# Optimization experiments

Hardware: AMD Instinct MI355X
Metric: run time of the kernel (lower is better)

Reference implementation:

```python
import jax, jax.numpy as jnp
import numpy as np
from jax import lax

B_SZ, D_SPEC, P, NC, MLP_D = 4096, 30, 9, 64, 64
L = P * P + 1  # 82 tokens (81 spiral + cls)


def _spiral_idx(patch=P):
    # Replicates Scan.forward's hardcoded assignments_map: center pixel, then
    # concentric rings (top row, right col, bottom row, left col), each of length 2r.
    cen = patch // 2
    rows, cols = [cen], [cen]
    for r in range(1, cen + 1):
        rows += [cen - r] * (2 * r); cols += list(range(cen - r + 1, cen + r + 1))
        rows += list(range(cen - r + 1, cen + r + 1)); cols += [cen + r] * (2 * r)
        rows += [cen + r] * (2 * r); cols += list(range(cen - r, cen + r))
        rows += list(range(cen - r, cen + r)); cols += [cen - r] * (2 * r)
    return np.asarray(rows), np.asarray(cols)

_ROWS, _COLS = _spiral_idx()


def _ln(x, g, b, eps=1e-5):
    m = x.mean(-1, keepdims=True)
    v = ((x - m) ** 2).mean(-1, keepdims=True)
    return (x - m) * lax.rsqrt(v + eps) * g + b


def _bn(x, g, b, m, v, nspatial, eps=1e-5):
    sh = (1, -1) + (1,) * nspatial
    return (x - m.reshape(sh)) * lax.rsqrt(v.reshape(sh) + eps) * g.reshape(sh) + b.reshape(sh)


def setup_inputs():
    key = jax.random.key(0)
    ks = iter(jax.random.split(key, 40))
    def rn(shape, s=0.1):
        return s * jax.random.normal(next(ks), shape, jnp.float32)
    return {
        "input_data": jax.random.normal(next(ks), (B_SZ, 1, D_SPEC, P, P), jnp.float32),
        "w3": rn((8, 1, 3, 3, 3)), "b3": rn((8,)),
        "g3": 1.0 + rn((8,)), "be3": rn((8,)), "m3": jnp.zeros((8,)), "v3": jnp.ones((8,)),
        "w2c": rn((NC, 8 * D_SPEC, 3, 3)), "b2c": rn((NC,)),
        "g2": 1.0 + rn((NC,)), "be2": rn((NC,)), "m2": jnp.zeros((NC,)), "v2": jnp.ones((NC,)),
        "pos_emb": rn((1, L, NC)), "cls_tok": rn((1, 1, NC)),
        "ln1_g": jnp.ones((NC,)), "ln1_b": jnp.zeros((NC,)),
        "Wb": rn((NC, NC)), "bb": rn((NC,)),
        "Wc": rn((NC, NC)), "bc": rn((NC,)),
        "Wd": rn((NC, NC)), "bd": rn((NC,)),
        "delta_p": rn((1, L, NC)), "A_p": rn((L, NC)),
        "Wst": rn((NC, NC)), "bst": rn((NC,)), "bias_st": rn((1, 1, NC)),
        "ln2_g": jnp.ones((NC,)), "ln2_b": jnp.zeros((NC,)),
        "Wm1": rn((NC, MLP_D)), "bm1": rn((MLP_D,)),
        "Wm2": rn((MLP_D, NC)), "bm2": rn((NC,)),
    }


def _forward(input_data, w3, b3, g3, be3, m3, v3, w2c, b2c, g2, be2, m2, v2,
             pos_emb, cls_tok, ln1_g, ln1_b, Wb, bb, Wc, bc, Wd, bd,
             delta_p, A_p, Wst, bst, bias_st, ln2_g, ln2_b, Wm1, bm1, Wm2, bm2):
    b = input_data.shape[0]
    # conv3d (SAME, k=3) + BN(eval) + ReLU
    h = lax.conv_general_dilated(input_data, w3, (1, 1, 1), [(1, 1)] * 3,
                                 dimension_numbers=("NCDHW", "OIDHW", "NCDHW"))
    h = jax.nn.relu(_bn(h + b3[None, :, None, None, None], g3, be3, m3, v3, 3))
    h = h.reshape(b, 8 * D_SPEC, P, P)  # 'b c h w y -> b (c h) w y'
    # conv2d (SAME, k=3) + BN(eval) + ReLU
    h = lax.conv_general_dilated(h, w2c, (1, 1), [(1, 1)] * 2,
                                 dimension_numbers=("NCHW", "OIHW", "NCHW"))
    h = jax.nn.relu(_bn(h + b2c[None, :, None, None], g2, be2, m2, v2, 2))
    # spiral scan gather: [B,C,H,W] -> [B,81,C]
    seq = jnp.transpose(h, (0, 2, 3, 1))[:, _ROWS, _COLS, :]
    tok = jnp.concatenate([jnp.broadcast_to(cls_tok, (b, 1, NC)), seq], axis=1) + pos_emb
    # (emb dropout = identity in eval)
    # --- Residual(LayerNormalize(S6_noC)) ---
    xn = _ln(tok, ln1_g, ln1_b)
    z = jax.nn.sigmoid(xn)
    B0 = xn @ Wb + bb
    C_ = xn @ Wc + bc
    sq = jnp.mean(xn, axis=1, keepdims=True)              # SToken squeeze [B,1,D]
    sq = jax.nn.sigmoid(jax.nn.relu(sq @ Wst + bst))
    T_ = (sq + bias_st) * xn                              # [B,L,D]
    delta = jax.nn.sigmoid(xn @ Wd + bd + delta_p)
    A_ = delta * A_p[None]                                # [B,L,D]
    Bx = delta * B0 * xn                                  # B_ * x fused
    def step(s, inp):
        a, bx, c, t = inp
        s = a * s + bx
        return s, c * s + t
    ins = (jnp.moveaxis(A_, 1, 0), jnp.moveaxis(Bx, 1, 0),
           jnp.moveaxis(C_, 1, 0), jnp.moveaxis(T_, 1, 0))  # [L,B,D]
    _, out = lax.scan(step, jnp.zeros((b, NC), xn.dtype), ins)
    tok = tok + jnp.moveaxis(out, 0, 1) * z               # residual
    # AdaptiveAvgPool1d(1) over seq + squeeze -> [B, D]
    pooled = tok.mean(axis=1)
    # --- Residual(LayerNormalize(MLP_Block)) (dropout = identity) ---
    yn = _ln(pooled, ln2_g, ln2_b)
    mlp = jax.nn.gelu(yn @ Wm1 + bm1, approximate=False) @ Wm2 + bm2
    return pooled + mlp


def reference(input_data, w3, b3, g3, be3, m3, v3, w2c, b2c, g2, be2, m2, v2,
              pos_emb, cls_tok, ln1_g, ln1_b, Wb, bb, Wc, bc, Wd, bd,
              delta_p, A_p, Wst, bst, bias_st, ln2_g, ln2_b, Wm1, bm1, Wm2, bm2):
    return _forward(input_data, w3, b3, g3, be3, m3, v3, w2c, b2c, g2, be2, m2, v2,
                    pos_emb, cls_tok, ln1_g, ln1_b, Wb, bb, Wc, bc, Wd, bd,
                    delta_p, A_p, Wst, bst, bias_st, ln2_g, ln2_b, Wm1, bm1, Wm2, bm2)
```

## Files before the change

kernel.cpp:

```cpp
#include <hip/hip_runtime.h>

typedef unsigned short u16;
typedef __attribute__((ext_vector_type(8))) short bf16x8;
typedef __attribute__((ext_vector_type(4))) float f32x4;
typedef __attribute__((ext_vector_type(4))) int i32x4;

#define DEV __device__ __forceinline__

DEV u16 f2bf(float f){
  unsigned u = __float_as_uint(f);
  u += 0x7fffu + ((u >> 16) & 1u);
  return (u16)(u >> 16);
}
DEV float bf2f(u16 h){ return __uint_as_float(((unsigned)h) << 16); }

DEV int spiral_t(int pix){
  int px = pix / 9, py = pix % 9;
  int dr = px - 4, dc = py - 4;
  int ar = dr < 0 ? -dr : dr, ac = dc < 0 ? -dc : dc;
  int r = ar > ac ? ar : ac;
  if (r == 0) return 0;
  int start = 1 + 4*r*(r-1);
  if (dr == -r && dc >= -r+1) return start + dc + r - 1;
  if (dc == r)  return start + 2*r + dr + r - 1;
  if (dr == r)  return start + 4*r + dc + r;
  return start + 6*r + dr + r;
}

__global__ __launch_bounds__(256) void k_wt(const float* __restrict__ w2c,
                                            const float* __restrict__ g2,
                                            const float* __restrict__ v2,
                                            u16* __restrict__ Wt2){
  int idx = blockIdx.x*256 + threadIdx.x;
  if (idx >= 72*64*32) return;
  int kk = idx & 31;
  int o  = (idx >> 5) & 63;
  int tile = idx >> 11;
  int dxy = tile >> 3;
  int chunk = tile & 7;
  int ch = chunk*32 + kk;
  float v = 0.f;
  if (ch < 240){
    float s2 = g2[o] * rsqrtf(v2[o] + 1e-5f);
    v = w2c[(o*240 + ch)*9 + dxy] * s2;
  }
  Wt2[idx] = f2bf(v);
}

__global__ __launch_bounds__(256) void k_conv3d(const float* __restrict__ x,
    const float* __restrict__ w3, const float* __restrict__ b3,
    const float* __restrict__ g3, const float* __restrict__ be3,
    const float* __restrict__ m3, const float* __restrict__ v3,
    u16* __restrict__ h1){
  __shared__ float tile[3872];
  __shared__ float wle[216];
  __shared__ float sc[8], sh[8];
  int b = blockIdx.x, tid = threadIdx.x;
  for (int i = tid; i < 3872; i += 256) tile[i] = 0.f;
  if (tid < 216) wle[tid] = w3[tid];
  if (tid < 8){
    float s = g3[tid]*rsqrtf(v3[tid]+1e-5f);
    sc[tid] = s;
    sh[tid] = (b3[tid]-m3[tid])*s + be3[tid];
  }
  __syncthreads();
  const float* xin = x + b*2430;
  for (int i = tid; i < 2430; i += 256){
    int dd = i / 81, rem = i % 81;
    int px = rem / 9, py = rem % 9;
    tile[(dd+1)*121 + (px+1)*11 + (py+1)] = xin[i];
  }
  __syncthreads();
  u16* hb = h1 + (size_t)b*19440;
  for (int p = tid; p < 2430; p += 256){
    int pix = p / 30, dd = p % 30;
    int px = pix / 9, py = pix % 9;
    const float* tp = tile + dd*121 + px*11 + py;
    float v[27];
    #pragma unroll
    for (int kd=0;kd<3;kd++)
      #pragma unroll
      for (int kx=0;kx<3;kx++)
        #pragma unroll
        for (int ky=0;ky<3;ky++)
          v[(kd*3+kx)*3+ky] = tp[kd*121 + kx*11 + ky];
    u16* hp = hb + pix*240 + dd;
    #pragma unroll
    for (int co=0;co<8;co++){
      float acc = 0.f;
      const float* wp = wle + co*27;
      #pragma unroll
      for (int q=0;q<27;q++) acc = fmaf(v[q], wp[q], acc);
      hp[co*30] = f2bf(fmaxf(acc*sc[co] + sh[co], 0.f));
    }
  }
}

__global__ __launch_bounds__(256, 2) void k_conv2d(const u16* __restrict__ h1,
    const u16* __restrict__ Wt2,
    const float* __restrict__ b2c, const float* __restrict__ g2,
    const float* __restrict__ be2, const float* __restrict__ m2,
    const float* __restrict__ v2,
    const float* __restrict__ pos_emb, const float* __restrict__ cls_tok,
    const float* __restrict__ ln1_g, const float* __restrict__ ln1_b,
    const float* __restrict__ Wst, const float* __restrict__ bst,
    const float* __restrict__ bias_st,
    u16* __restrict__ xn, float* __restrict__ tsum, float* __restrict__ sqs){
  __shared__ __align__(16) char smem[80848];
  const int ZROW = 80352;
  int tid = threadIdx.x;
  int wv = tid >> 6, ln = tid & 63;
  int lq = ln >> 4, lr = ln & 15;
  int img0 = blockIdx.x*2;
  size_t grow0 = (size_t)img0*81;

  for (int r = tid; r < 162; r += 256)
    *(i32x4*)(smem + r*496 + 480) = (i32x4){0,0,0,0};
  if (tid < 31) *(i32x4*)(smem + ZROW + tid*16) = (i32x4){0,0,0,0};
  {
    const u16* src = h1 + grow0*240;
    for (int idx = tid; idx < 162*30; idx += 256){
      int r = idx / 30, c = idx % 30;
      *(i32x4*)(smem + r*496 + c*16) = *(const i32x4*)(src + idx*8);
    }
  }
  __syncthreads();

  f32x4 acc[3][4];
  #pragma unroll
  for (int i=0;i<3;i++)
    #pragma unroll
    for (int j=0;j<4;j++) acc[i][j] = (f32x4){0.f,0.f,0.f,0.f};

  int bln = lr*32 + lq*8;

#define CALCADDR(TAP, A0, A1, A13)                                              \
  { int dx = (TAP)/3 - 1, dy = (TAP)%3 - 1;                                     \
    _Pragma("unroll")                                                           \
    for (int rt=0;rt<3;rt++){                                                   \
      int row = (wv*3+rt)*16 + lr;                                              \
      int pix = row % 81;                                                       \
      int px = pix/9, py = pix%9;                                               \
      int px2 = px + dx, py2 = py + dy;                                         \
      bool valid = (row < 162) && ((unsigned)px2 < 9u) && ((unsigned)py2 < 9u); \
      int nrow = (row - pix) + px2*9 + py2;                                     \
      int base = valid ? nrow*496 : ZROW;                                       \
      A0[rt]  = base + lq*16;                                                   \
      A1[rt]  = base + 64 + lq*16;                                              \
      A13[rt] = (lq == 3) ? ZROW : (A1[rt] + 384);                              \
    } }

#define LOADB(TAP, C, B)                                                        \
    { const u16* Bt_ = Wt2 + (TAP)*16384 + bln;                                 \
      _Pragma("unroll")                                                         \
      for (int kk=0;kk<2;kk++)                                                  \
        _Pragma("unroll")                                                       \
        for (int j=0;j<4;j++)                                                   \
          B[kk][j] = *(const bf16x8*)(Bt_ + ((C)*2+kk)*2048 + j*512); }

#define LOADA(C, SA0, SA1, SA13, A0, A1)                                        \
    { _Pragma("unroll")                                                         \
      for (int rt=0;rt<3;rt++){                                                 \
        A0[rt] = *(const bf16x8*)(smem + SA0[rt] + (C)*128);                    \
        A1[rt] = *(const bf16x8*)(smem + ((C)==3 ? SA13[rt]                     \
                                                 : SA1[rt] + (C)*128)); } }

#define DOMFMA(B, A0, A1)                                                       \
    { _Pragma("unroll")                                                         \
      for (int rt=0;rt<3;rt++)                                                  \
        _Pragma("unroll")                                                       \
        for (int j=0;j<4;j++)                                                   \
          acc[rt][j] = __builtin_amdgcn_mfma_f32_16x16x32_bf16(A0[rt], B[0][j], acc[rt][j], 0, 0, 0); \
      _Pragma("unroll")                                                         \
      for (int rt=0;rt<3;rt++)                                                  \
        _Pragma("unroll")                                                       \
        for (int j=0;j<4;j++)                                                   \
          acc[rt][j] = __builtin_amdgcn_mfma_f32_16x16x32_bf16(A1[rt], B[1][j], acc[rt][j], 0, 0, 0); }

  int aC0[3], aC1[3], aC13[3];
  int aN0[3], aN1[3], aN13[3];
  bf16x8 bX[2][4], bY[2][4], aX0[3], aX1[3], aY0[3], aY1[3];

  CALCADDR(0, aC0, aC1, aC13);
  LOADB(0, 0, bX); LOADA(0, aC0, aC1, aC13, aX0, aX1);
  LOADB(0, 1, bY); LOADA(1, aC0, aC1, aC13, aY0, aY1);

  for (int tap = 0; tap < 9; tap++){
    int ntap = (tap < 8) ? tap + 1 : 8;
    DOMFMA(bX, aX0, aX1);
    LOADB(tap, 2, bX); LOADA(2, aC0, aC1, aC13, aX0, aX1);
    DOMFMA(bY, aY0, aY1);
    LOADB(tap, 3, bY); LOADA(3, aC0, aC1, aC13, aY0, aY1);
    CALCADDR(ntap, aN0, aN1, aN13);
    DOMFMA(bX, aX0, aX1);
    LOADB(ntap, 0, bX); LOADA(0, aN0, aN1, aN13, aX0, aX1);
    DOMFMA(bY, aY0, aY1);
    LOADB(ntap, 1, bY); LOADA(1, aN0, aN1, aN13, aY0, aY1);
    #pragma unroll
    for (int rt=0;rt<3;rt++){ aC0[rt]=aN0[rt]; aC1[rt]=aN1[rt]; aC13[rt]=aN13[rt]; }
  }
#undef CALCADDR
#undef LOADB
#undef LOADA
#undef DOMFMA

  __syncthreads();

  float t2c[4], lg[4], lb[4];
  #pragma unroll
  for (int j=0;j<4;j++){
    int col = j*16 + lr;
    float s2 = g2[col]*rsqrtf(v2[col]+1e-5f);
    t2c[j] = (b2c[col]-m2[col])*s2 + be2[col];
    lg[j] = ln1_g[col]; lb[j] = ln1_b[col];
  }

  float st0[4]={0,0,0,0}, st1[4]={0,0,0,0};
  float sx0[4]={0,0,0,0}, sx1[4]={0,0,0,0};

  #pragma unroll
  for (int rt=0;rt<3;rt++){
    #pragma unroll
    for (int e=0;e<4;e++){
      int row = (wv*3+rt)*16 + lq*4 + e;
      if (row < 162){
        int im = (row >= 81);
        int pix = row - im*81;
        int tsp = spiral_t(pix);
        const float* pe = pos_emb + (1+tsp)*64;
        float y[4], m1 = 0.f, m2v = 0.f;
        #pragma unroll
        for (int j=0;j<4;j++){
          y[j] = fmaxf(acc[rt][j][e] + t2c[j], 0.f) + pe[j*16+lr];
          m1 += y[j]; m2v = fmaf(y[j], y[j], m2v);
        }
        #pragma unroll
        for (int off=1; off<16; off<<=1){
          m1  += __shfl_xor(m1,  off, 64);
          m2v += __shfl_xor(m2v, off, 64);
        }
        float mean = m1*(1.f/64.f);
        float var  = m2v*(1.f/64.f) - mean*mean;
        float rs = rsqrtf(var + 1e-5f);
        u16* dst = xn + ((size_t)(img0+im)*82 + 1 + tsp)*64;
        #pragma unroll
        for (int j=0;j<4;j++){
          float xnv = (y[j]-mean)*rs*lg[j] + lb[j];
          dst[j*16+lr] = f2bf(xnv);
          if (im == 0){ st0[j] += y[j]; sx0[j] += xnv; }
          else        { st1[j] += y[j]; sx1[j] += xnv; }
        }
      }
    }
  }

  #pragma unroll
  for (int j=0;j<4;j++){
    st0[j] += __shfl_xor(st0[j],16,64); st0[j] += __shfl_xor(st0[j],32,64);
    st1[j] += __shfl_xor(st1[j],16,64); st1[j] += __shfl_xor(st1[j],32,64);
    sx0[j] += __shfl_xor(sx0[j],16,64); sx0[j] += __shfl_xor(sx0[j],32,64);
    sx1[j] += __shfl_xor(sx1[j],16,64); sx1[j] += __shfl_xor(sx1[j],32,64);
  }
  float* partT = (float*)smem;
  float* partX = (float*)(smem + 2048);
  float* xsumL = (float*)(smem + 4096);
  if (lq == 0){
    #pragma unroll
    for (int j=0;j<4;j++){
      partT[wv*128 +       j*16+lr] = st0[j];
      partT[wv*128 + 64  + j*16+lr] = st1[j];
      partX[wv*128 +       j*16+lr] = sx0[j];
      partX[wv*128 + 64  + j*16+lr] = sx1[j];
    }
  }
  __syncthreads();
  if (tid < 128){
    int im = tid >> 6, d = tid & 63;
    float tt = partT[im*64+d] + partT[128+im*64+d] + partT[256+im*64+d] + partT[384+im*64+d];
    float xx = partX[im*64+d] + partX[128+im*64+d] + partX[256+im*64+d] + partX[384+im*64+d];
    float clsv = cls_tok[d] + pos_emb[d];
    float c1 = clsv, c2 = clsv*clsv;
    #pragma unroll
    for (int off=1; off<64; off<<=1){ c1 += __shfl_xor(c1, off, 64); c2 += __shfl_xor(c2, off, 64); }
    float cm = c1*(1.f/64.f), cv = c2*(1.f/64.f) - cm*cm;
    float cxn = (clsv - cm)*rsqrtf(cv + 1e-5f)*ln1_g[d] + ln1_b[d];
    xn[((size_t)(img0+im)*82)*64 + d] = f2bf(cxn);
    tsum[(size_t)(img0+im)*64 + d] = tt + clsv;
    xsumL[im*64 + d] = (xx + cxn) * (1.f/82.f);
  }
  __syncthreads();
  if (tid < 128){
    int im = tid >> 6, d = tid & 63;
    float a = bst[d];
    for (int k=0;k<64;k++) a = fmaf(xsumL[im*64+k], Wst[k*64+d], a);
    a = fmaxf(a, 0.f);
    a = 1.f/(1.f + __expf(-a));
    sqs[(size_t)(img0+im)*64 + d] = a + bias_st[d];
  }
}

__global__ __launch_bounds__(256, 1) void k_bcd(const u16* __restrict__ xn,
    const float* __restrict__ Wb, const float* __restrict__ Wc, const float* __restrict__ Wd,
    const float* __restrict__ bbv, const float* __restrict__ bcv,
    const float* __restrict__ bdv,
    const float* __restrict__ delta_p, const float* __restrict__ A_p,
    u16* __restrict__ Ax, u16* __restrict__ Bxx, u16* __restrict__ Cx){
  __shared__ char At[16384];
  int tid = threadIdx.x;
  int wv = tid >> 6, ln = tid & 63;
  int lq = ln >> 4, lr = ln & 15;
  size_t r0 = (size_t)blockIdx.x * 128;

  {
    int row = tid >> 1, hh = tid & 1;
    const char* src = (const char*)xn + (r0 + row)*128 + hh*64;
    #pragma unroll
    for (int c=0;c<4;c++){
      i32x4 v = *(const i32x4*)(src + c*16);
      *(i32x4*)(At + row*128 + ((hh*64 + c*16) ^ ((row&7)<<4))) = v;
    }
  }

  bf16x8 bfr[2][12];
  #pragma unroll
  for (int kk=0;kk<2;kk++)
    #pragma unroll
    for (int j=0;j<12;j++){
      int c = j*16 + lr;
      const float* W = (c < 64) ? Wb : ((c < 128) ? Wc : Wd);
      int cc = c & 63;
      int k0 = kk*32 + lq*8;
      bf16x8 f;
      #pragma unroll
      for (int e=0;e<8;e++) f[e] = (short)f2bf(W[(k0+e)*64 + cc]);
      bfr[kk][j] = f;
    }
  __syncthreads();

  f32x4 acc[2][12];
  #pragma unroll
  for (int i=0;i<2;i++)
    #pragma unroll
    for (int j=0;j<12;j++) acc[i][j] = (f32x4){0.f,0.f,0.f,0.f};

  #pragma unroll
  for (int kk=0;kk<2;kk++){
    bf16x8 afr[2];
    #pragma unroll
    for (int i=0;i<2;i++){
      int row = wv*32 + i*16 + lr;
      afr[i] = *(const bf16x8*)(At + row*128 + ((kk*64 + lq*16) ^ ((row&7)<<4)));
    }
    #pragma unroll
    for (int i=0;i<2;i++)
      #pragma unroll
      for (int j=0;j<12;j++)
        acc[i][j] = __builtin_amdgcn_mfma_f32_16x16x32_bf16(afr[i], bfr[kk][j], acc[i][j], 0, 0, 0);
  }

  #pragma unroll
  for (int i=0;i<2;i++){
    #pragma unroll
    for (int e=0;e<4;e++){
      int row = wv*32 + i*16 + lq*4 + e;
      unsigned rr = (unsigned)(r0 + row);
      unsigned t = rr % 82u;
      #pragma unroll
      for (int j=0;j<4;j++){
        int d = j*16 + lr;
        float B0 = acc[i][j][e]   + bbv[d];
        float Cv = acc[i][j+4][e] + bcv[d];
        float Dr = acc[i][j+8][e] + bdv[d] + delta_p[t*64+d];
        float D  = 1.f/(1.f + __expf(-Dr));
        int byte = j*32 + lr*2;
        float xv = bf2f(*(const u16*)(At + row*128 + (byte ^ ((row&7)<<4))));
        size_t o = (size_t)rr*64 + d;
        Ax[o]  = f2bf(D * A_p[t*64+d]);
        Bxx[o] = f2bf(D * B0 * xv);
        Cx[o]  = f2bf(Cv);
      }
    }
  }
}

__global__ __launch_bounds__(256) void k_scan(const u16* __restrict__ xn,
    const u16* __restrict__ Ax, const u16* __restrict__ Bxx, const u16* __restrict__ Cx,
    const float* __restrict__ tsum, const float* __restrict__ sqs,
    const float* __restrict__ ln2_g, const float* __restrict__ ln2_b,
    const float* __restrict__ Wm1, const float* __restrict__ bm1,
    const float* __restrict__ Wm2, const float* __restrict__ bm2,
    float* __restrict__ out){
  int tid = threadIdx.x, wv = tid >> 6, d = tid & 63;
  int b = blockIdx.x*4 + wv;
  float sq = sqs[b*64 + d];
  float s = 0.f, racc = 0.f;
  size_t base = (size_t)b*82*64 + d;
  #pragma unroll 2
  for (int t = 0; t < 82; t++){
    float a  = bf2f(Ax[base]);
    float bx = bf2f(Bxx[base]);
    float c  = bf2f(Cx[base]);
    float xv = bf2f(xn[base]);
    s = fmaf(a, s, bx);
    float o = fmaf(c, s, sq*xv);
    float z = 1.f/(1.f + __expf(-xv));
    racc = fmaf(o, z, racc);
    base += 64;
  }
  float pooled = (tsum[b*64 + d] + racc) * (1.f/82.f);
  float s1 = pooled, s2v = pooled*pooled;
  #pragma unroll
  for (int off=32; off>0; off>>=1){ s1 += __shfl_xor(s1, off, 64); s2v += __shfl_xor(s2v, off, 64); }
  float mean = s1*(1.f/64.f), var = s2v*(1.f/64.f) - mean*mean;
  float yn = (pooled - mean)*rsqrtf(var + 1e-5f)*ln2_g[d] + ln2_b[d];
  float a1 = bm1[d];
  for (int k=0;k<64;k++) a1 = fmaf(__shfl(yn, k, 64), Wm1[k*64+d], a1);
  float hg = 0.5f*a1*(1.f + erff(a1*0.70710678118654752f));
  float a2 = bm2[d];
  for (int k=0;k<64;k++) a2 = fmaf(__shfl(hg, k, 64), Wm2[k*64+d], a2);
  out[b*64 + d] = pooled + a2;
}

extern "C" void kernel_launch(void* const* d_in, const int* in_sizes, int n_in,
                              void* d_out, int out_size, void* d_ws, size_t ws_size,
                              hipStream_t stream){
  const float* x       = (const float*)d_in[0];
  const float* w3      = (const float*)d_in[1];
  const float* b3      = (const float*)d_in[2];
  const float* g3      = (const float*)d_in[3];
  const float* be3     = (const float*)d_in[4];
  const float* m3      = (const float*)d_in[5];
  const float* v3      = (const float*)d_in[6];
  const float* w2c     = (const float*)d_in[7];
  const float* b2c     = (const float*)d_in[8];
  const float* g2      = (const float*)d_in[9];
  const float* be2     = (const float*)d_in[10];
  const float* m2      = (const float*)d_in[11];
  const float* v2      = (const float*)d_in[12];
  const float* pos_emb = (const float*)d_in[13];
  const float* cls_tok = (const float*)d_in[14];
  const float* ln1_g   = (const float*)d_in[15];
  const float* ln1_b   = (const float*)d_in[16];
  const float* Wb      = (const float*)d_in[17];
  const float* bbv     = (const float*)d_in[18];
  const float* Wc      = (const float*)d_in[19];
  const float* bc      = (const float*)d_in[20];
  const float* Wd      = (const float*)d_in[21];
  const float* bd      = (const float*)d_in[22];
  const float* delta_p = (const float*)d_in[23];
  const float* A_p     = (const float*)d_in[24];
  const float* Wst     = (const float*)d_in[25];
  const float* bst     = (const float*)d_in[26];
  const float* bias_st = (const float*)d_in[27];
  const float* ln2_g   = (const float*)d_in[28];
  const float* ln2_b   = (const float*)d_in[29];
  const float* Wm1     = (const float*)d_in[30];
  const float* bm1     = (const float*)d_in[31];
  const float* Wm2     = (const float*)d_in[32];
  const float* bm2     = (const float*)d_in[33];

  char* ws = (char*)d_ws;
  u16*   h1   = (u16*)ws;
  u16*   Wt2  = (u16*)(ws + 159252480);
  u16*   xnb  = (u16*)(ws + 159571968);
  float* tsum = (float*)(ws + 202563584);
  float* sqs  = (float*)(ws + 203612160);
  u16*   Ax   = (u16*)ws;
  u16*   Cx   = (u16*)(ws + 42991616);
  u16*   Bxx  = (u16*)(ws + 85983232);

  k_wt    <<<576,  256, 0, stream>>>(w2c, g2, v2, Wt2);
  k_conv3d<<<4096, 256, 0, stream>>>(x, w3, b3, g3, be3, m3, v3, h1);
  k_conv2d<<<2048, 256, 0, stream>>>(h1, Wt2, b2c, g2, be2, m2, v2,
                                     pos_emb, cls_tok, ln1_g, ln1_b,
                                     Wst, bst, bias_st, xnb, tsum, sqs);
  k_bcd   <<<2624, 256, 0, stream>>>(xnb, Wb, Wc, Wd, bbv, bc, bd, delta_p, A_p,
                                     Ax, Bxx, Cx);
  k_scan  <<<1024, 256, 0, stream>>>(xnb, Ax, Bxx, Cx, tsum, sqs,
                                     ln2_g, ln2_b, Wm1, bm1, Wm2, bm2, (float*)d_out);
}
```

Baseline: 412.4 us.

## Triple-buffer conv weight fragments, prioritize MFMA waves, split squeeze matvec

The implicit-GEMM conv2d main loop now rotates three B-fragment register buffers instead of two, so global weight loads for later K-chunks are issued earlier and have more MFMA work to hide behind. The loop is unrolled over groups of three taps, and the first weight loads are issued before the shared-memory fill. MFMA blocks are wrapped in s_setprio to favour waves doing matrix work. The squeeze matvec now uses all 256 threads, with each thread summing half of the k range and a shuffle combining the halves. The extra buffer raises VGPR pressure, which could hurt the 2-waves-per-SIMD occupancy target.

```diff
diff --git a/kernel.cpp b/kernel.cpp
--- a/kernel.cpp
+++ b/kernel.cpp
@@ -114,6 +114,21 @@
   int img0 = blockIdx.x*2;
   size_t grow0 = (size_t)img0*81;
 
+  int bln = lr*32 + lq*8;
+
+#define LOADB(TAP, C, B)                                                        \
+    { const u16* Bt_ = Wt2 + (TAP)*16384 + bln;                                 \
+      _Pragma("unroll")                                                         \
+      for (int kk=0;kk<2;kk++)                                                  \
+        _Pragma("unroll")                                                       \
+        for (int j=0;j<4;j++)                                                   \
+          B[kk][j] = *(const bf16x8*)(Bt_ + ((C)*2+kk)*2048 + j*512); }
+
+  bf16x8 bB0[2][4], bB1[2][4], bB2[2][4];
+  LOADB(0, 0, bB0);
+  LOADB(0, 1, bB1);
+  LOADB(0, 2, bB2);
+
   for (int r = tid; r < 162; r += 256)
     *(i32x4*)(smem + r*496 + 480) = (i32x4){0,0,0,0};
   if (tid < 31) *(i32x4*)(smem + ZROW + tid*16) = (i32x4){0,0,0,0};
@@ -131,8 +146,6 @@
   for (int i=0;i<3;i++)
     #pragma unroll
     for (int j=0;j<4;j++) acc[i][j] = (f32x4){0.f,0.f,0.f,0.f};
-
-  int bln = lr*32 + lq*8;
 
 #define CALCADDR(TAP, A0, A1, A13)                                              \
   { int dx = (TAP)/3 - 1, dy = (TAP)%3 - 1;                                     \
@@ -150,14 +163,6 @@
       A13[rt] = (lq == 3) ? ZROW : (A1[rt] + 384);                              \
     } }
 
-#define LOADB(TAP, C, B)                                                        \
-    { const u16* Bt_ = Wt2 + (TAP)*16384 + bln;                                 \
-      _Pragma("unroll")                                                         \
-      for (int kk=0;kk<2;kk++)                                                  \
-        _Pragma("unroll")                                                       \
-        for (int j=0;j<4;j++)                                                   \
-          B[kk][j] = *(const bf16x8*)(Bt_ + ((C)*2+kk)*2048 + j*512); }
-
 #define LOADA(C, SA0, SA1, SA13, A0, A1)                                        \
     { _Pragma("unroll")                                                         \
       for (int rt=0;rt<3;rt++){                                                 \
@@ -166,7 +171,8 @@
                                                  : SA1[rt] + (C)*128)); } }
 
 #define DOMFMA(B, A0, A1)                                                       \
-    { _Pragma("unroll")                                                         \
+    { __builtin_amdgcn_s_setprio(1);                                            \
+      _Pragma("unroll")                                                         \
       for (int rt=0;rt<3;rt++)                                                  \
         _Pragma("unroll")                                                       \
         for (int j=0;j<4;j++)                                                   \
@@ -175,34 +181,41 @@
       for (int rt=0;rt<3;rt++)                                                  \
         _Pragma("unroll")                                                       \
         for (int j=0;j<4;j++)                                                   \
-          acc[rt][j] = __builtin_amdgcn_mfma_f32_16x16x32_bf16(A1[rt], B[1][j], acc[rt][j], 0, 0, 0); }
+          acc[rt][j] = __builtin_amdgcn_mfma_f32_16x16x32_bf16(A1[rt], B[1][j], acc[rt][j], 0, 0, 0); \
+      __builtin_amdgcn_s_setprio(0); }
+
+#define TAPBODY(TAPV, BA, BB, BC)                                               \
+  { int ntap_ = (TAPV) < 8 ? (TAPV)+1 : 8;                                      \
+    DOMFMA(BA, aAX0, aAX1);                                                     \
+    LOADB((TAPV), 3, BA); LOADA(2, aC0, aC1, aC13, aAX0, aAX1);                 \
+    DOMFMA(BB, aAY0, aAY1);                                                     \
+    LOADB(ntap_, 0, BB); CALCADDR(ntap_, aN0, aN1, aN13);                       \
+    LOADA(3, aC0, aC1, aC13, aAY0, aAY1);                                       \
+    DOMFMA(BC, aAX0, aAX1);                                                     \
+    LOADB(ntap_, 1, BC); LOADA(0, aN0, aN1, aN13, aAX0, aAX1);                  \
+    DOMFMA(BA, aAY0, aAY1);                                                     \
+    LOADB(ntap_, 2, BA); LOADA(1, aN0, aN1, aN13, aAY0, aAY1);                  \
+    _Pragma("unroll")                                                           \
+    for (int rt=0;rt<3;rt++){ aC0[rt]=aN0[rt]; aC1[rt]=aN1[rt]; aC13[rt]=aN13[rt]; } }
 
   int aC0[3], aC1[3], aC13[3];
   int aN0[3], aN1[3], aN13[3];
-  bf16x8 bX[2][4], bY[2][4], aX0[3], aX1[3], aY0[3], aY1[3];
+  bf16x8 aAX0[3], aAX1[3], aAY0[3], aAY1[3];
 
   CALCADDR(0, aC0, aC1, aC13);
-  LOADB(0, 0, bX); LOADA(0, aC0, aC1, aC13, aX0, aX1);
-  LOADB(0, 1, bY); LOADA(1, aC0, aC1, aC13, aY0, aY1);
-
-  for (int tap = 0; tap < 9; tap++){
-    int ntap = (tap < 8) ? tap + 1 : 8;
-    DOMFMA(bX, aX0, aX1);
-    LOADB(tap, 2, bX); LOADA(2, aC0, aC1, aC13, aX0, aX1);
-    DOMFMA(bY, aY0, aY1);
-    LOADB(tap, 3, bY); LOADA(3, aC0, aC1, aC13, aY0, aY1);
-    CALCADDR(ntap, aN0, aN1, aN13);
-    DOMFMA(bX, aX0, aX1);
-    LOADB(ntap, 0, bX); LOADA(0, aN0, aN1, aN13, aX0, aX1);
-    DOMFMA(bY, aY0, aY1);
-    LOADB(ntap, 1, bY); LOADA(1, aN0, aN1, aN13, aY0, aY1);
-    #pragma unroll
-    for (int rt=0;rt<3;rt++){ aC0[rt]=aN0[rt]; aC1[rt]=aN1[rt]; aC13[rt]=aN13[rt]; }
+  LOADA(0, aC0, aC1, aC13, aAX0, aAX1);
+  LOADA(1, aC0, aC1, aC13, aAY0, aAY1);
+
+  for (int t3 = 0; t3 < 9; t3 += 3){
+    TAPBODY(t3+0, bB0, bB1, bB2);
+    TAPBODY(t3+1, bB1, bB2, bB0);
+    TAPBODY(t3+2, bB2, bB0, bB1);
   }
 #undef CALCADDR
 #undef LOADB
 #undef LOADA
 #undef DOMFMA
+#undef TAPBODY
 
   __syncthreads();
 
@@ -289,13 +302,20 @@
     xsumL[im*64 + d] = (xx + cxn) * (1.f/82.f);
   }
   __syncthreads();
-  if (tid < 128){
-    int im = tid >> 6, d = tid & 63;
-    float a = bst[d];
-    for (int k=0;k<64;k++) a = fmaf(xsumL[im*64+k], Wst[k*64+d], a);
-    a = fmaxf(a, 0.f);
-    a = 1.f/(1.f + __expf(-a));
-    sqs[(size_t)(img0+im)*64 + d] = a + bias_st[d];
+  {
+    int im = tid >> 7, d2 = tid & 127;
+    int d = d2 >> 1, half = d2 & 1;
+    float a = 0.f;
+    int k0 = half*32;
+    #pragma unroll
+    for (int k=0;k<32;k++) a = fmaf(xsumL[im*64 + k0+k], Wst[(k0+k)*64+d], a);
+    a += __shfl_xor(a, 1, 64);
+    if (half == 0){
+      a += bst[d];
+      a = fmaxf(a, 0.f);
+      a = 1.f/(1.f + __expf(-a));
+      sqs[(size_t)(img0+im)*64 + d] = a + bias_st[d];
+    }
   }
 }
 
```

After: 407.0 us. Within noise of the previous version (-1.3%).

## Split conv2d K across wave pairs with LDS reduction and setprio MFMA groups

Applied to the files above, without the earlier changes.

Restructures the conv2d MFMA loop so each pair of waves covers 96 rows (6 row tiles) and splits the 4 K-chunks of each tap between the two waves. Each wave then loads only half the weight fragments per tap, and the partial accumulators are reduced through shared memory before the epilogue. The loop interleaves per-tile LDS loads with MFMA groups and raises wave priority around the MFMAs. The final Wst matvec now uses all 256 threads, each summing half of K and combining with a shuffle. In exchange the kernel carries twice as many accumulator registers and an extra LDS exchange with barriers, which may hurt occupancy at 2 blocks per CU.

```diff
diff --git a/kernel.cpp b/kernel.cpp
--- a/kernel.cpp
+++ b/kernel.cpp
@@ -111,8 +111,24 @@
   int tid = threadIdx.x;
   int wv = tid >> 6, ln = tid & 63;
   int lq = ln >> 4, lr = ln & 15;
+  int p = wv >> 1, q = wv & 1;
   int img0 = blockIdx.x*2;
   size_t grow0 = (size_t)img0*81;
+
+  int bln = lr*32 + lq*8;
+  int c0 = q*2, c1 = q*2 + 1;
+
+#define LOADB(TAP, C, B)                                                        \
+    { const u16* Bt_ = Wt2 + (TAP)*16384 + bln;                                 \
+      _Pragma("unroll")                                                         \
+      for (int kk=0;kk<2;kk++)                                                  \
+        _Pragma("unroll")                                                       \
+        for (int j=0;j<4;j++)                                                   \
+          B[kk][j] = *(const bf16x8*)(Bt_ + ((C)*2+kk)*2048 + j*512); }
+
+  bf16x8 bA[2][4], bB[2][4];
+  LOADB(0, c0, bA);
+  LOADB(0, c1, bB);
 
   for (int r = tid; r < 162; r += 256)
     *(i32x4*)(smem + r*496 + 480) = (i32x4){0,0,0,0};
@@ -126,84 +142,90 @@
   }
   __syncthreads();
 
-  f32x4 acc[3][4];
-  #pragma unroll
-  for (int i=0;i<3;i++)
+  f32x4 acc[6][4];
+  #pragma unroll
+  for (int i=0;i<6;i++)
     #pragma unroll
     for (int j=0;j<4;j++) acc[i][j] = (f32x4){0.f,0.f,0.f,0.f};
 
-  int bln = lr*32 + lq*8;
-
-#define CALCADDR(TAP, A0, A1, A13)                                              \
+  int aC0[6], aC1[6];
+  bf16x8 afr[6][2];
+
+#define CALCADDR(TAP)                                                           \
   { int dx = (TAP)/3 - 1, dy = (TAP)%3 - 1;                                     \
     _Pragma("unroll")                                                           \
-    for (int rt=0;rt<3;rt++){                                                   \
-      int row = (wv*3+rt)*16 + lr;                                              \
+    for (int rt=0;rt<6;rt++){                                                   \
+      int row = p*96 + rt*16 + lr;                                              \
       int pix = row % 81;                                                       \
       int px = pix/9, py = pix%9;                                               \
       int px2 = px + dx, py2 = py + dy;                                         \
       bool valid = (row < 162) && ((unsigned)px2 < 9u) && ((unsigned)py2 < 9u); \
       int nrow = (row - pix) + px2*9 + py2;                                     \
       int base = valid ? nrow*496 : ZROW;                                       \
-      A0[rt]  = base + lq*16;                                                   \
-      A1[rt]  = base + 64 + lq*16;                                              \
-      A13[rt] = (lq == 3) ? ZROW : (A1[rt] + 384);                              \
+      aC0[rt] = base + lq*16;                                                   \
+      aC1[rt] = base + 64 + lq*16;                                              \
     } }
 
-#define LOADB(TAP, C, B)                                                        \
-    { const u16* Bt_ = Wt2 + (TAP)*16384 + bln;                                 \
-      _Pragma("unroll")                                                         \
-      for (int kk=0;kk<2;kk++)                                                  \
+#define LOADA1(RT, C)                                                           \
+    { afr[RT][0] = *(const bf16x8*)(smem + aC0[RT] + (C)*128);                  \
+      int a1a_ = ((C)==3) ? ((lq==3) ? ZROW : aC1[RT] + 384)                    \
+                          : (aC1[RT] + (C)*128);                                \
+      afr[RT][1] = *(const bf16x8*)(smem + a1a_); }
+
+#define GROUP(B, NC)                                                            \
+    { _Pragma("unroll")                                                         \
+      for (int rt=0;rt<6;rt++){                                                 \
+        __builtin_amdgcn_s_setprio(1);                                          \
         _Pragma("unroll")                                                       \
         for (int j=0;j<4;j++)                                                   \
-          B[kk][j] = *(const bf16x8*)(Bt_ + ((C)*2+kk)*2048 + j*512); }
-
-#define LOADA(C, SA0, SA1, SA13, A0, A1)                                        \
-    { _Pragma("unroll")                                                         \
-      for (int rt=0;rt<3;rt++){                                                 \
-        A0[rt] = *(const bf16x8*)(smem + SA0[rt] + (C)*128);                    \
-        A1[rt] = *(const bf16x8*)(smem + ((C)==3 ? SA13[rt]                     \
-                                                 : SA1[rt] + (C)*128)); } }
-
-#define DOMFMA(B, A0, A1)                                                       \
-    { _Pragma("unroll")                                                         \
-      for (int rt=0;rt<3;rt++)                                                  \
+          acc[rt][j] = __builtin_amdgcn_mfma_f32_16x16x32_bf16(afr[rt][0], B[0][j], acc[rt][j], 0, 0, 0); \
         _Pragma("unroll")                                                       \
         for (int j=0;j<4;j++)                                                   \
-          acc[rt][j] = __builtin_amdgcn_mfma_f32_16x16x32_bf16(A0[rt], B[0][j], acc[rt][j], 0, 0, 0); \
-      _Pragma("unroll")                                                         \
-      for (int rt=0;rt<3;rt++)                                                  \
-        _Pragma("unroll")                                                       \
-        for (int j=0;j<4;j++)                                                   \
-          acc[rt][j] = __builtin_amdgcn_mfma_f32_16x16x32_bf16(A1[rt], B[1][j], acc[rt][j], 0, 0, 0); }
-
-  int aC0[3], aC1[3], aC13[3];
-  int aN0[3], aN1[3], aN13[3];
-  bf16x8 bX[2][4], bY[2][4], aX0[3], aX1[3], aY0[3], aY1[3];
-
-  CALCADDR(0, aC0, aC1, aC13);
-  LOADB(0, 0, bX); LOADA(0, aC0, aC1, aC13, aX0, aX1);
-  LOADB(0, 1, bY); LOADA(1, aC0, aC1, aC13, aY0, aY1);
+          acc[rt][j] = __builtin_amdgcn_mfma_f32_16x16x32_bf16(afr[rt][1], B[1][j], acc[rt][j], 0, 0, 0); \
+        __builtin_amdgcn_s_setprio(0);                                          \
+        LOADA1(rt, NC);                                                         \
+      } }
+
+  CALCADDR(0);
+  #pragma unroll
+  for (int rt=0;rt<6;rt++){ LOADA1(rt, c0); }
 
   for (int tap = 0; tap < 9; tap++){
     int ntap = (tap < 8) ? tap + 1 : 8;
-    DOMFMA(bX, aX0, aX1);
-    LOADB(tap, 2, bX); LOADA(2, aC0, aC1, aC13, aX0, aX1);
-    DOMFMA(bY, aY0, aY1);
-    LOADB(tap, 3, bY); LOADA(3, aC0, aC1, aC13, aY0, aY1);
-    CALCADDR(ntap, aN0, aN1, aN13);
-    DOMFMA(bX, aX0, aX1);
-    LOADB(ntap, 0, bX); LOADA(0, aN0, aN1, aN13, aX0, aX1);
-    DOMFMA(bY, aY0, aY1);
-    LOADB(ntap, 1, bY); LOADA(1, aN0, aN1, aN13, aY0, aY1);
-    #pragma unroll
-    for (int rt=0;rt<3;rt++){ aC0[rt]=aN0[rt]; aC1[rt]=aN1[rt]; aC13[rt]=aN13[rt]; }
+    GROUP(bA, c1);
+    LOADB(ntap, c0, bA);
+    CALCADDR(ntap);
+    GROUP(bB, c0);
+    LOADB(ntap, c1, bB);
   }
 #undef CALCADDR
 #undef LOADB
-#undef LOADA
-#undef DOMFMA
-
+#undef LOADA1
+#undef GROUP
+
+  __syncthreads();
+  float* ex = (float*)smem;
+  int rtw0 = q ? 0 : 3;
+  #pragma unroll
+  for (int k=0;k<3;k++){
+    int rt = rtw0 + k;
+    #pragma unroll
+    for (int e=0;e<4;e++)
+      #pragma unroll
+      for (int j=0;j<4;j++)
+        ex[p*6144 + (rt*16 + lq*4 + e)*64 + j*16 + lr] = acc[rt][j][e];
+  }
+  __syncthreads();
+  int rtr0 = q ? 3 : 0;
+  #pragma unroll
+  for (int k=0;k<3;k++){
+    int rt = rtr0 + k;
+    #pragma unroll
+    for (int e=0;e<4;e++)
+      #pragma unroll
+      for (int j=0;j<4;j++)
+        acc[rt][j][e] += ex[p*6144 + (rt*16 + lq*4 + e)*64 + j*16 + lr];
+  }
   __syncthreads();
 
   float t2c[4], lg[4], lb[4];
@@ -219,10 +241,11 @@
   float sx0[4]={0,0,0,0}, sx1[4]={0,0,0,0};
 
   #pragma unroll
-  for (int rt=0;rt<3;rt++){
+  for (int k=0;k<3;k++){
+    int rt = rtr0 + k;
     #pragma unroll
     for (int e=0;e<4;e++){
-      int row = (wv*3+rt)*16 + lq*4 + e;
+      int row = p*96 + rt*16 + lq*4 + e;
       if (row < 162){
         int im = (row >= 81);
         int pix = row - im*81;
@@ -279,23 +302,30 @@
     float tt = partT[im*64+d] + partT[128+im*64+d] + partT[256+im*64+d] + partT[384+im*64+d];
     float xx = partX[im*64+d] + partX[128+im*64+d] + partX[256+im*64+d] + partX[384+im*64+d];
     float clsv = cls_tok[d] + pos_emb[d];
-    float c1 = clsv, c2 = clsv*clsv;
-    #pragma unroll
-    for (int off=1; off<64; off<<=1){ c1 += __shfl_xor(c1, off, 64); c2 += __shfl_xor(c2, off, 64); }
-    float cm = c1*(1.f/64.f), cv = c2*(1.f/64.f) - cm*cm;
+    float c1v = clsv, c2v = clsv*clsv;
+    #pragma unroll
+    for (int off=1; off<64; off<<=1){ c1v += __shfl_xor(c1v, off, 64); c2v += __shfl_xor(c2v, off, 64); }
+    float cm = c1v*(1.f/64.f), cv = c2v*(1.f/64.f) - cm*cm;
     float cxn = (clsv - cm)*rsqrtf(cv + 1e-5f)*ln1_g[d] + ln1_b[d];
     xn[((size_t)(img0+im)*82)*64 + d] = f2bf(cxn);
     tsum[(size_t)(img0+im)*64 + d] = tt + clsv;
     xsumL[im*64 + d] = (xx + cxn) * (1.f/82.f);
   }
   __syncthreads();
-  if (tid < 128){
-    int im = tid >> 6, d = tid & 63;
-    float a = bst[d];
-    for (int k=0;k<64;k++) a = fmaf(xsumL[im*64+k], Wst[k*64+d], a);
-    a = fmaxf(a, 0.f);
-    a = 1.f/(1.f + __expf(-a));
-    sqs[(size_t)(img0+im)*64 + d] = a + bias_st[d];
+  {
+    int im = tid >> 7, d2 = tid & 127;
+    int d = d2 >> 1, half = d2 & 1;
+    float a = 0.f;
+    int k0 = half*32;
+    #pragma unroll
+    for (int k=0;k<32;k++) a = fmaf(xsumL[im*64 + k0+k], Wst[(k0+k)*64+d], a);
+    a += __shfl_xor(a, 1, 64);
+    if (half == 0){
+      a += bst[d];
+      a = fmaxf(a, 0.f);
+      a = 1.f/(1.f + __expf(-a));
+      sqs[(size_t)(img0+im)*64 + d] = a + bias_st[d];
+    }
   }
 }
 
```

Result: slower. 611.1 us (+48.2%).
